# Kernel optimization log

Measured on AMD Instinct MI355X. Metric: run time of the kernel, lower is better.

Reference implementation:

```python
import jax, jax.numpy as jnp
import numpy as np


def setup_inputs() -> dict:
    key = jax.random.key(0)
    k1, k2 = jax.random.split(key)
    B, T_enc, T_dec, D = 8, 2048, 2048, 128
    encoder_hidden_states = jax.random.normal(k1, (B, T_enc, D), dtype=jnp.float32)
    decoder_hidden_states = jax.random.normal(k2, (B, T_dec, D), dtype=jnp.float32)
    return {"encoder_hidden_states": encoder_hidden_states,
            "decoder_hidden_states": decoder_hidden_states}


def reference(encoder_hidden_states, decoder_hidden_states):
    # dot_product[b,q,k] = dec[b,q,:] . enc[b,k,:]
    dot_product = jnp.einsum("bqd,bkd->bqk", decoder_hidden_states, encoder_hidden_states)
    # attn_scores[b,q,d] = sum_k dot_product[b,q,k] * enc[b,k,d]
    # (the torch code materializes the 4D broadcast; this is the same math as a bmm)
    attn_scores = jnp.einsum("bqk,bkd->bqd", dot_product, encoder_hidden_states)
    return attn_scores
```

## Files before the change

kernel.cpp:

```cpp
#include <hip/hip_runtime.h>

#define BB 8
#define TT 2048
#define DD 128
#define CH 32

typedef __attribute__((ext_vector_type(8))) short bf16x8;
typedef __attribute__((ext_vector_type(4))) float f32x4;
typedef unsigned short u16;

static __device__ __forceinline__ float bf2f(u16 u) {
    union { unsigned int i; float f; } v; v.i = ((unsigned int)u) << 16; return v.f;
}
static __device__ __forceinline__ u16 f2bf(float f) {
    union { float f; unsigned int i; } v; v.f = f;
    unsigned int x = v.i;
    return (u16)((x + 0x7FFFu + ((x >> 16) & 1u)) >> 16);
}


__global__ __launch_bounds__(1024, 4) void gram_mfma(const float* __restrict__ enc,
                                                     u16* __restrict__ P) {
    const int bid  = blockIdx.x;
    const int b    = bid & 7;
    const int c    = bid >> 3;
    const int t    = threadIdx.x;
    const int wave = t >> 6, lane = t & 63, quad = lane >> 4, ln = lane & 15;

    __shared__ __align__(16) u16 Gt[DD * 64];

    const int d = t & 127, kg = t >> 7;
    {
        const float* src = enc + ((size_t)b * TT + (size_t)c * 64) * DD;
        union { u16 o[8]; uint4 q; } cv;
        #pragma unroll
        for (int i = 0; i < 8; ++i) cv.o[i] = f2bf(src[(kg * 8 + i) * DD + d]);
        *(uint4*)&Gt[d * 64 + ((kg ^ (d & 7)) << 3)] = cv.q;
    }
    __syncthreads();

    const int mt = wave >> 1, parity = wave & 1;
    f32x4 acc[4];
    #pragma unroll
    for (int s = 0; s < 4; ++s) acc[s] = (f32x4){0.f, 0.f, 0.f, 0.f};

    #pragma unroll
    for (int ks = 0; ks < 2; ++ks) {
        const int g = ((ks * 4 + quad) ^ (ln & 7)) << 3;
        const bf16x8 af = *(const bf16x8*)&Gt[(mt * 16 + ln) * 64 + g];
        #pragma unroll
        for (int s = 0; s < 4; ++s) {
            const int nt = parity + 2 * s;
            const bf16x8 bf = *(const bf16x8*)&Gt[(nt * 16 + ln) * 64 + g];
            acc[s] = __builtin_amdgcn_mfma_f32_16x16x32_bf16(af, bf, acc[s], 0, 0, 0);
        }
    }

    u16* Pb = P + ((size_t)c * BB + b) * (DD * DD);
    #pragma unroll
    for (int s = 0; s < 4; ++s) {
        const int nt = parity + 2 * s;
        u16 o[4];
        #pragma unroll
        for (int r = 0; r < 4; ++r) o[r] = f2bf(acc[s][r]);
        *(ushort4*)&Pb[(mt * 8 + nt) * 256 + ln * 16 + quad * 4] = *(const ushort4*)o;
    }
}

__global__ __launch_bounds__(128) void gram_reduce(const u16* __restrict__ P,
                                                   u16* __restrict__ G) {
    const int g = blockIdx.x * 128 + threadIdx.x;
    const ushort4* Pu = (const ushort4*)P;
    const int stride = BB * DD * DD / 4;
    float sx = 0.f, sy = 0.f, sz = 0.f, sw = 0.f;
    #pragma unroll
    for (int c = 0; c < CH; ++c) {
        const ushort4 v = Pu[(size_t)c * stride + g];
        sx += bf2f(v.x); sy += bf2f(v.y); sz += bf2f(v.z); sw += bf2f(v.w);
    }
    ushort4 o; o.x = f2bf(sx); o.y = f2bf(sy); o.z = f2bf(sz); o.w = f2bf(sw);
    ((ushort4*)G)[g] = o;
}

__global__ __launch_bounds__(1024, 4) void apply_mfma(const float* __restrict__ dec,
                                                      const u16* __restrict__ G,
                                                      float* __restrict__ out) {
    const int bid  = blockIdx.x;
    const int b    = bid & 7;
    const int c    = bid >> 3;
    const int t    = threadIdx.x;
    const int wave = t >> 6, lane = t & 63, quad = lane >> 4, ln = lane & 15;

    __shared__ __align__(16) u16 Gs[DD * DD];

    const int rowt = wave & 3, dgrp = wave >> 2;
    const float* drow = dec + ((size_t)b * TT + (size_t)c * 64 + rowt * 16 + ln) * DD
                        + quad * 8;
    bf16x8 dfrag[4];
    #pragma unroll
    for (int ks = 0; ks < 4; ++ks) {
        const float4 d0 = *(const float4*)(drow + ks * 32);
        const float4 d1 = *(const float4*)(drow + ks * 32 + 4);
        union { u16 o[8]; bf16x8 v; } u;
        u.o[0] = f2bf(d0.x); u.o[1] = f2bf(d0.y); u.o[2] = f2bf(d0.z); u.o[3] = f2bf(d0.w);
        u.o[4] = f2bf(d1.x); u.o[5] = f2bf(d1.y); u.o[6] = f2bf(d1.z); u.o[7] = f2bf(d1.w);
        dfrag[ks] = u.v;
    }

    {
        const uint4* Gq = (const uint4*)(G + (size_t)b * DD * DD);
        #pragma unroll
        for (int i = 0; i < 2; ++i)
            ((uint4*)Gs)[i * 1024 + t] = Gq[i * 1024 + t];
    }
    __syncthreads();

    f32x4 oacc[2];
    #pragma unroll
    for (int dtl = 0; dtl < 2; ++dtl) oacc[dtl] = (f32x4){0.f, 0.f, 0.f, 0.f};

    #pragma unroll
    for (int ks = 0; ks < 4; ++ks) {
        const int mtk  = ks * 2 + (quad >> 1);
        const int boff = ln * 16 + (quad & 1) * 8;
        #pragma unroll
        for (int dtl = 0; dtl < 2; ++dtl) {
            const int dt = dgrp * 2 + dtl;
            const bf16x8 bbf = *(const bf16x8*)&Gs[(mtk * 8 + dt) * 256 + boff];
            oacc[dtl] = __builtin_amdgcn_mfma_f32_16x16x32_bf16(
                dfrag[ks], bbf, oacc[dtl], 0, 0, 0);
        }
    }

    float* ob = out + ((size_t)b * TT + (size_t)c * 64 + rowt * 16) * DD;
    #pragma unroll
    for (int dtl = 0; dtl < 2; ++dtl) {
        const int dcol = (dgrp * 2 + dtl) * 16 + ln;
        #pragma unroll
        for (int r = 0; r < 4; ++r)
            ob[(quad * 4 + r) * DD + dcol] = oacc[dtl][r];
    }
}

extern "C" void kernel_launch(void* const* d_in, const int* in_sizes, int n_in,
                              void* d_out, int out_size, void* d_ws, size_t ws_size,
                              hipStream_t stream) {
    const float* enc = (const float*)d_in[0];
    const float* dec = (const float*)d_in[1];
    float* out = (float*)d_out;

    u16* P = (u16*)d_ws;
    u16* G = (u16*)((char*)d_ws + (size_t)CH * BB * DD * DD * sizeof(u16));

    gram_mfma<<<dim3(CH * BB), 1024, 0, stream>>>(enc, P);
    gram_reduce<<<BB * DD * DD / 4 / 128, 128, 0, stream>>>(P, G);
    apply_mfma<<<dim3(CH * BB), 1024, 0, stream>>>(dec, G, out);
}
```

Measured before the change: 80.17 us.

## Fuse gram reduction into apply kernel and halve gram chunk count

Removes the separate gram_reduce kernel; each apply block now sums the partial Gram matrices for its batch directly into shared memory before the MFMA apply. The gram kernel now processes 128 rows per block in two 64-row tiles with register prefetch of the second tile, halving the number of partials to reduce. This saves a launch and the G round trip, but every apply block redundantly reads all 16 partials for its batch, adding L2 traffic.

```diff
diff --git a/kernel.cpp b/kernel.cpp
--- a/kernel.cpp
+++ b/kernel.cpp
@@ -3,7 +3,7 @@
 #define BB 8
 #define TT 2048
 #define DD 128
-#define CH 32
+#define CH 16
 
 typedef __attribute__((ext_vector_type(8))) short bf16x8;
 typedef __attribute__((ext_vector_type(4))) float f32x4;
@@ -27,17 +27,14 @@
     const int t    = threadIdx.x;
     const int wave = t >> 6, lane = t & 63, quad = lane >> 4, ln = lane & 15;
 
-    __shared__ __align__(16) u16 Gt[DD * 64];
+    __shared__ __align__(16) u16 Gt[2][DD * 64];
 
     const int d = t & 127, kg = t >> 7;
-    {
-        const float* src = enc + ((size_t)b * TT + (size_t)c * 64) * DD;
-        union { u16 o[8]; uint4 q; } cv;
-        #pragma unroll
-        for (int i = 0; i < 8; ++i) cv.o[i] = f2bf(src[(kg * 8 + i) * DD + d]);
-        *(uint4*)&Gt[d * 64 + ((kg ^ (d & 7)) << 3)] = cv.q;
-    }
-    __syncthreads();
+    const float* src = enc + ((size_t)b * TT + (size_t)c * 128) * DD;
+
+    float pf[8];
+    #pragma unroll
+    for (int i = 0; i < 8; ++i) pf[i] = src[(kg * 8 + i) * DD + d];
 
     const int mt = wave >> 1, parity = wave & 1;
     f32x4 acc[4];
@@ -45,14 +42,29 @@
     for (int s = 0; s < 4; ++s) acc[s] = (f32x4){0.f, 0.f, 0.f, 0.f};
 
     #pragma unroll
-    for (int ks = 0; ks < 2; ++ks) {
-        const int g = ((ks * 4 + quad) ^ (ln & 7)) << 3;
-        const bf16x8 af = *(const bf16x8*)&Gt[(mt * 16 + ln) * 64 + g];
+    for (int tt = 0; tt < 2; ++tt) {
+        {
+            union { u16 o[8]; uint4 q; } cv;
+            #pragma unroll
+            for (int i = 0; i < 8; ++i) cv.o[i] = f2bf(pf[i]);
+            *(uint4*)&Gt[tt][d * 64 + ((kg ^ (d & 7)) << 3)] = cv.q;
+        }
+        if (tt == 0) {
+            #pragma unroll
+            for (int i = 0; i < 8; ++i) pf[i] = src[(64 + kg * 8 + i) * DD + d];
+        }
+        __syncthreads();
+
         #pragma unroll
-        for (int s = 0; s < 4; ++s) {
-            const int nt = parity + 2 * s;
-            const bf16x8 bf = *(const bf16x8*)&Gt[(nt * 16 + ln) * 64 + g];
-            acc[s] = __builtin_amdgcn_mfma_f32_16x16x32_bf16(af, bf, acc[s], 0, 0, 0);
+        for (int ks = 0; ks < 2; ++ks) {
+            const int g = ((ks * 4 + quad) ^ (ln & 7)) << 3;
+            const bf16x8 af = *(const bf16x8*)&Gt[tt][(mt * 16 + ln) * 64 + g];
+            #pragma unroll
+            for (int s = 0; s < 4; ++s) {
+                const int nt = parity + 2 * s;
+                const bf16x8 bf = *(const bf16x8*)&Gt[tt][(nt * 16 + ln) * 64 + g];
+                acc[s] = __builtin_amdgcn_mfma_f32_16x16x32_bf16(af, bf, acc[s], 0, 0, 0);
+            }
         }
     }
 
@@ -67,34 +79,19 @@
     }
 }
 
-__global__ __launch_bounds__(128) void gram_reduce(const u16* __restrict__ P,
-                                                   u16* __restrict__ G) {
-    const int g = blockIdx.x * 128 + threadIdx.x;
-    const ushort4* Pu = (const ushort4*)P;
-    const int stride = BB * DD * DD / 4;
-    float sx = 0.f, sy = 0.f, sz = 0.f, sw = 0.f;
-    #pragma unroll
-    for (int c = 0; c < CH; ++c) {
-        const ushort4 v = Pu[(size_t)c * stride + g];
-        sx += bf2f(v.x); sy += bf2f(v.y); sz += bf2f(v.z); sw += bf2f(v.w);
-    }
-    ushort4 o; o.x = f2bf(sx); o.y = f2bf(sy); o.z = f2bf(sz); o.w = f2bf(sw);
-    ((ushort4*)G)[g] = o;
-}
-
-__global__ __launch_bounds__(1024, 4) void apply_mfma(const float* __restrict__ dec,
-                                                      const u16* __restrict__ G,
-                                                      float* __restrict__ out) {
+__global__ __launch_bounds__(1024, 4) void reduce_apply(const float* __restrict__ dec,
+                                                        const u16* __restrict__ P,
+                                                        float* __restrict__ out) {
     const int bid  = blockIdx.x;
     const int b    = bid & 7;
-    const int c    = bid >> 3;
+    const int q    = bid >> 3;
     const int t    = threadIdx.x;
     const int wave = t >> 6, lane = t & 63, quad = lane >> 4, ln = lane & 15;
 
     __shared__ __align__(16) u16 Gs[DD * DD];
 
     const int rowt = wave & 3, dgrp = wave >> 2;
-    const float* drow = dec + ((size_t)b * TT + (size_t)c * 64 + rowt * 16 + ln) * DD
+    const float* drow = dec + ((size_t)b * TT + (size_t)q * 64 + rowt * 16 + ln) * DD
                         + quad * 8;
     bf16x8 dfrag[4];
     #pragma unroll
@@ -107,11 +104,25 @@
         dfrag[ks] = u.v;
     }
 
-    {
-        const uint4* Gq = (const uint4*)(G + (size_t)b * DD * DD);
+    #pragma unroll
+    for (int i = 0; i < 2; ++i) {
+        const int g = i * 1024 + t;
+        const uint4* Pu = (const uint4*)P;
+        float s[8];
         #pragma unroll
-        for (int i = 0; i < 2; ++i)
-            ((uint4*)Gs)[i * 1024 + t] = Gq[i * 1024 + t];
+        for (int j = 0; j < 8; ++j) s[j] = 0.f;
+        #pragma unroll
+        for (int c2 = 0; c2 < CH; ++c2) {
+            const uint4 v = Pu[((size_t)c2 * BB + b) * 2048 + g];
+            s[0] += bf2f((u16)(v.x & 0xffff)); s[1] += bf2f((u16)(v.x >> 16));
+            s[2] += bf2f((u16)(v.y & 0xffff)); s[3] += bf2f((u16)(v.y >> 16));
+            s[4] += bf2f((u16)(v.z & 0xffff)); s[5] += bf2f((u16)(v.z >> 16));
+            s[6] += bf2f((u16)(v.w & 0xffff)); s[7] += bf2f((u16)(v.w >> 16));
+        }
+        union { u16 o[8]; uint4 qv; } cv;
+        #pragma unroll
+        for (int j = 0; j < 8; ++j) cv.o[j] = f2bf(s[j]);
+        ((uint4*)Gs)[g] = cv.qv;
     }
     __syncthreads();
 
@@ -132,7 +143,7 @@
         }
     }
 
-    float* ob = out + ((size_t)b * TT + (size_t)c * 64 + rowt * 16) * DD;
+    float* ob = out + ((size_t)b * TT + (size_t)q * 64 + rowt * 16) * DD;
     #pragma unroll
     for (int dtl = 0; dtl < 2; ++dtl) {
         const int dcol = (dgrp * 2 + dtl) * 16 + ln;
@@ -150,9 +161,7 @@
     float* out = (float*)d_out;
 
     u16* P = (u16*)d_ws;
-    u16* G = (u16*)((char*)d_ws + (size_t)CH * BB * DD * DD * sizeof(u16));
 
     gram_mfma<<<dim3(CH * BB), 1024, 0, stream>>>(enc, P);
-    gram_reduce<<<BB * DD * DD / 4 / 128, 128, 0, stream>>>(P, G);
-    apply_mfma<<<dim3(CH * BB), 1024, 0, stream>>>(dec, G, out);
+    reduce_apply<<<dim3(32 * BB), 1024, 0, stream>>>(dec, P, out);
 }
```

Result: no change. 81.00 us (+1.0%).
